# Optimization experiments

Hardware: AMD Instinct MI355X
Metric: run time of the kernel (lower is better)

## Reference

```python
import jax, jax.numpy as jnp
import numpy as np

N = 8192        # points
M = 131072      # query-key pairs (edges)
C_IN = 512
H = 8           # heads
D = 64          # head_channels
BINS = 48
BIN_SIZE = 0.05


def setup_inputs() -> dict:
    key = jax.random.key(0)
    ks = jax.random.split(key, 8)
    x_F = jax.random.normal(ks[0], (N, C_IN), dtype=jnp.float32)
    x_C = jax.random.uniform(ks[1], (N, 3), dtype=jnp.float32)
    qk_pair_idxs = jax.random.randint(ks[2], (2, M), 0, N, dtype=jnp.int64)
    W_qkv = jax.random.normal(ks[3], (C_IN, 3 * H * D), dtype=jnp.float32) * 0.02
    b_qkv = jnp.zeros((3 * H * D,), dtype=jnp.float32)
    q_tables = jax.random.normal(ks[4], (3, BINS, H, D), dtype=jnp.float32) * 0.02
    k_tables = jax.random.normal(ks[5], (3, BINS, H, D), dtype=jnp.float32) * 0.02
    v_tables = jax.random.normal(ks[6], (3, BINS, H, D), dtype=jnp.float32) * 0.02
    return {"x_F": x_F, "x_C": x_C, "qk_pair_idxs": qk_pair_idxs,
            "W_qkv": W_qkv, "b_qkv": b_qkv,
            "q_tables": q_tables, "k_tables": k_tables, "v_tables": v_tables}


def reference(x_F, x_C, qk_pair_idxs, W_qkv, b_qkv, q_tables, k_tables, v_tables):
    n = x_F.shape[0]
    qkv = (x_F @ W_qkv + b_qkv).reshape(n, 3, H, D)
    q = qkv[:, 0] * (D ** -0.5)   # scale folded into queries, as in the module
    k = qkv[:, 1]
    v = qkv[:, 2]
    qi = qk_pair_idxs[0]
    ki = qk_pair_idxs[1]
    # quantized relative coordinates -> table bin indices [M,3]
    rel = (x_C[qi] - x_C[ki]) / BIN_SIZE + BINS / 2
    idx = jnp.clip(rel.astype(jnp.int32), 0, BINS - 1)
    # precompute per-point, per-axis, per-bin table dot products [N,3,BINS,H]
    q_dot = jnp.einsum('nhd,abhd->nabh', q, q_tables)
    k_dot = jnp.einsum('nhd,abhd->nabh', k, k_tables)
    # content logits [M,H]
    logits = jnp.einsum('mhd,mhd->mh', q[qi], k[ki])
    for a in range(3):  # fixed xyz axes
        logits = logits + q_dot[qi, a, idx[:, a]] + k_dot[ki, a, idx[:, a]]
    # scatter softmax over query index (per head)
    seg_max = jax.ops.segment_max(logits, qi, num_segments=n)
    e = jnp.exp(logits - seg_max[qi])
    denom = jax.ops.segment_sum(e, qi, num_segments=n)
    attn = e / denom[qi]  # [M,H]
    # value-side relative position bias, summed over axes [M,H,D]
    vt = v_tables[0, idx[:, 0]] + v_tables[1, idx[:, 1]] + v_tables[2, idx[:, 2]]
    contrib = attn[:, :, None] * (v[ki] + vt)            # [M,H,D]
    agg = jax.ops.segment_sum(contrib, qi, num_segments=n)  # [N,H,D]
    return agg.reshape(n, H * D)
```

## Files before the change

### kernel.cpp

```cpp
#include <hip/hip_runtime.h>
#include <hip/hip_bf16.h>
#include <stdint.h>

#define N_PTS 8192
#define M_EDGES 131072
#define CIN 512
#define QKV_COLS 1536

typedef __bf16 bf16x8 __attribute__((ext_vector_type(8)));
typedef float f32x4 __attribute__((ext_vector_type(4)));

#define GAS __attribute__((address_space(1)))
#define LAS __attribute__((address_space(3)))

__device__ __forceinline__ void gload_lds16(const void* g, void* l) {
  __builtin_amdgcn_global_load_lds((const GAS void*)g, (LAS void*)l, 16, 0, 0);
}

__global__ void cast_a(const float* __restrict__ x, __bf16* __restrict__ a) {
  int i = blockIdx.x * blockDim.x + threadIdx.x;
  int base = i * 4;
  if (base < N_PTS * CIN) {
    float4 v = *(const float4*)(x + base);
    a[base + 0] = (__bf16)v.x;
    a[base + 1] = (__bf16)v.y;
    a[base + 2] = (__bf16)v.z;
    a[base + 3] = (__bf16)v.w;
  }
}

__global__ void cast_bt(const float* __restrict__ w, __bf16* __restrict__ bt) {
  __shared__ float tile[32][33];
  int bk = blockIdx.x, bn = blockIdx.y;
  int x = threadIdx.x & 31, y = threadIdx.x >> 5;
#pragma unroll
  for (int j = 0; j < 4; j++) {
    int r = y + j * 8;
    tile[r][x] = w[(size_t)(bk * 32 + r) * QKV_COLS + bn * 32 + x];
  }
  __syncthreads();
#pragma unroll
  for (int j = 0; j < 4; j++) {
    int r = y + j * 8;
    bt[(size_t)(bn * 32 + r) * CIN + bk * 32 + x] = (__bf16)tile[x][r];
  }
}

__global__ void cast_tables(const float* __restrict__ qt, const float* __restrict__ kt,
                            const float* __restrict__ vt, __bf16* __restrict__ qtb,
                            __bf16* __restrict__ ktb, __bf16* __restrict__ vtb) {
  int i = blockIdx.x * 256 + threadIdx.x;
  if (i >= 3 * 48 * 512) return;
  int d = i & 63, h = (i >> 6) & 7, ab = i >> 9;
  int po = (h * 144 + ab) * 64 + d;
  qtb[po] = (__bf16)qt[i];
  ktb[po] = (__bf16)kt[i];
  vtb[i] = (__bf16)vt[i];
}

__global__ __launch_bounds__(256) void gemm_qkv(const __bf16* __restrict__ A,
                                                const __bf16* __restrict__ BT,
                                                const float* __restrict__ bias,
                                                __bf16* __restrict__ qb,
                                                __bf16* __restrict__ kb,
                                                __bf16* __restrict__ vb) {
  __shared__ __align__(16) char At[128 * 32 * 2];
  __shared__ __align__(16) char Bt[128 * 32 * 2];
  int tid = threadIdx.x;
  int w = tid >> 6, l = tid & 63;
  int bm = blockIdx.x, bn = blockIdx.y;
  int wm = w & 1, wn = w >> 1;
  f32x4 acc[4][4] = {};
  const char* Ab = (const char*)A;
  const char* Bb = (const char*)BT;

  for (int kt = 0; kt < 16; kt++) {
#pragma unroll
    for (int r = 0; r < 2; r++) {
      int flat = r * 4096 + w * 1024 + l * 16;
      int row = flat >> 6, colb = flat & 63;
      gload_lds16(Ab + ((size_t)(bm * 128 + row) * CIN + kt * 32) * 2 + colb,
                  At + r * 4096 + w * 1024);
      gload_lds16(Bb + ((size_t)(bn * 128 + row) * CIN + kt * 32) * 2 + colb,
                  Bt + r * 4096 + w * 1024);
    }
    __syncthreads();
    bf16x8 af[4], bfr[4];
    int lr = l & 15;
    int lk = (l >> 4) * 16;
#pragma unroll
    for (int mf = 0; mf < 4; mf++) af[mf] = *(const bf16x8*)(At + (wm * 64 + mf * 16 + lr) * 64 + lk);
#pragma unroll
    for (int nf = 0; nf < 4; nf++) bfr[nf] = *(const bf16x8*)(Bt + (wn * 64 + nf * 16 + lr) * 64 + lk);
#pragma unroll
    for (int mf = 0; mf < 4; mf++)
#pragma unroll
      for (int nf = 0; nf < 4; nf++)
        acc[mf][nf] = __builtin_amdgcn_mfma_f32_16x16x32_bf16(af[mf], bfr[nf], acc[mf][nf], 0, 0, 0);
    __syncthreads();
  }

  int lr = l & 15, lg = l >> 4;
#pragma unroll
  for (int mf = 0; mf < 4; mf++) {
#pragma unroll
    for (int nf = 0; nf < 4; nf++) {
      int gc = bn * 128 + wn * 64 + nf * 16 + lr;
      float b = bias[gc];
      int which = gc >> 9;
      int col = gc & 511;
      __bf16* dst = which == 0 ? qb : (which == 1 ? kb : vb);
      float scale = which == 0 ? 0.125f : 1.0f;
#pragma unroll
      for (int j = 0; j < 4; j++) {
        int gr = bm * 128 + wm * 64 + mf * 16 + lg * 4 + j;
        dst[(size_t)gr * 512 + col] = (__bf16)((acc[mf][nf][j] + b) * scale);
      }
    }
  }
}

__global__ __launch_bounds__(256) void table_dot(const __bf16* __restrict__ src,
                                                 const __bf16* __restrict__ tab,
                                                 __bf16* __restrict__ out) {
  __shared__ __align__(16) char As[128 * 128];
  __shared__ __align__(16) char Bs[144 * 128];
  int nt = blockIdx.x, h = blockIdx.y;
  int tid = threadIdx.x, w = tid >> 6, l = tid & 63;
  const char* sb = (const char*)src;
  const char* tb = (const char*)tab + (size_t)h * 144 * 128;
#pragma unroll
  for (int p = 0; p < 4; p++) {
    int flat = p * 4096 + w * 1024 + l * 16;
    int row = flat >> 7, colb = flat & 127;
    gload_lds16(sb + (size_t)(nt * 128 + row) * 1024 + h * 128 + colb, As + p * 4096 + w * 1024);
    gload_lds16(tb + flat, Bs + p * 4096 + w * 1024);
  }
  if (w < 2) {
    int flat = 16384 + w * 1024 + l * 16;
    gload_lds16(tb + flat, Bs + 16384 + w * 1024);
  }
  __syncthreads();

  f32x4 acc[2][9] = {};
  int lr = l & 15, lk = (l >> 4) * 16;
#pragma unroll
  for (int ks = 0; ks < 2; ks++) {
    bf16x8 af[2], bf[9];
#pragma unroll
    for (int mf = 0; mf < 2; mf++)
      af[mf] = *(const bf16x8*)(As + (w * 32 + mf * 16 + lr) * 128 + ks * 64 + lk);
#pragma unroll
    for (int nf = 0; nf < 9; nf++)
      bf[nf] = *(const bf16x8*)(Bs + (nf * 16 + lr) * 128 + ks * 64 + lk);
#pragma unroll
    for (int mf = 0; mf < 2; mf++)
#pragma unroll
      for (int nf = 0; nf < 9; nf++)
        acc[mf][nf] = __builtin_amdgcn_mfma_f32_16x16x32_bf16(af[mf], bf[nf], acc[mf][nf], 0, 0, 0);
  }

  int lg = l >> 4;
#pragma unroll
  for (int mf = 0; mf < 2; mf++)
#pragma unroll
    for (int nf = 0; nf < 9; nf++)
#pragma unroll
      for (int j = 0; j < 4; j++) {
        int n = nt * 128 + w * 32 + mf * 16 + lg * 4 + j;
        int ab = nf * 16 + lr;
        out[(size_t)n * 1152 + ab * 8 + h] = (__bf16)acc[mf][nf][j];
      }
}

__global__ void edge_setup(const int* __restrict__ pairs, const float* __restrict__ xc,
                           int* __restrict__ qi_a, int* __restrict__ ki_a,
                           unsigned* __restrict__ bins, int* __restrict__ cnt) {
  int m = blockIdx.x * blockDim.x + threadIdx.x;
  if (m >= M_EDGES) return;
  int qi = pairs[m], ki = pairs[M_EDGES + m];
  unsigned pb = 0;
#pragma unroll
  for (int a = 0; a < 3; a++) {
    float rel = (xc[qi * 3 + a] - xc[ki * 3 + a]) / 0.05f + 24.0f;
    int b = (int)rel;
    b = b < 0 ? 0 : (b > 47 ? 47 : b);
    pb |= (unsigned)b << (6 * a);
  }
  qi_a[m] = qi;
  ki_a[m] = ki;
  bins[m] = pb;
  atomicAdd(&cnt[qi], 1);
}

__global__ __launch_bounds__(256) void scan_kernel(const int* __restrict__ cnt,
                                                   int* __restrict__ off,
                                                   int* __restrict__ cursor) {
  __shared__ int wsum[4];
  int tid = threadIdx.x, lane = tid & 63, w = tid >> 6;
  int local[32];
  int s = 0;
#pragma unroll
  for (int i = 0; i < 8; i++) {
    int4 v = ((const int4*)cnt)[tid * 8 + i];
    local[i * 4 + 0] = v.x; local[i * 4 + 1] = v.y;
    local[i * 4 + 2] = v.z; local[i * 4 + 3] = v.w;
    s += v.x + v.y + v.z + v.w;
  }
  int incl = s;
#pragma unroll
  for (int d = 1; d < 64; d <<= 1) {
    int t = __shfl_up(incl, d, 64);
    if (lane >= d) incl += t;
  }
  if (lane == 63) wsum[w] = incl;
  __syncthreads();
  int woff = 0;
#pragma unroll
  for (int j = 0; j < 4; j++) woff += (j < w) ? wsum[j] : 0;
  int run = woff + incl - s;
  int base = tid * 32;
#pragma unroll
  for (int i = 0; i < 32; i++) {
    off[base + i] = run;
    cursor[base + i] = run;
    run += local[i];
  }
  if (tid == 255) off[N_PTS] = run;
}

__global__ void scatter_k(const int* __restrict__ qi_a, const int* __restrict__ ki_a,
                          const unsigned* __restrict__ bins, int* __restrict__ cursor,
                          int* __restrict__ qi_s, int* __restrict__ ki_s,
                          unsigned* __restrict__ bins_s) {
  int m = blockIdx.x * blockDim.x + threadIdx.x;
  if (m < M_EDGES) {
    int qi = qi_a[m];
    int pos = atomicAdd(&cursor[qi], 1);
    qi_s[pos] = qi;
    ki_s[pos] = ki_a[m];
    bins_s[pos] = bins[m];
  }
}

__global__ void edge_bias(const int* __restrict__ qi_s, const int* __restrict__ ki_s,
                          const unsigned* __restrict__ bins_s, const __bf16* __restrict__ qdot,
                          const __bf16* __restrict__ kdot, float* __restrict__ eb) {
  int t = blockIdx.x * 256 + threadIdx.x;
  int e = t >> 3, h = t & 7;
  if (e >= M_EDGES) return;
  int qi = qi_s[e], ki = ki_s[e];
  unsigned pb = bins_s[e];
  int a0 = ((int)(pb & 63)) * 8 + h;
  int a1 = (48 + (int)((pb >> 6) & 63)) * 8 + h;
  int a2 = (96 + (int)((pb >> 12) & 63)) * 8 + h;
  const __bf16* qd = qdot + (size_t)qi * 1152;
  const __bf16* kd = kdot + (size_t)ki * 1152;
  eb[t] = (float)qd[a0] + (float)qd[a1] + (float)qd[a2] +
          (float)kd[a0] + (float)kd[a1] + (float)kd[a2];
}

__global__ __launch_bounds__(512) void attn_kernel(
    const __bf16* __restrict__ qb, const __bf16* __restrict__ kb,
    const __bf16* __restrict__ vb, const __bf16* __restrict__ vtb,
    const float* __restrict__ eb, const int* __restrict__ off,
    const int* __restrict__ ki_s, const unsigned* __restrict__ bins_s,
    float* __restrict__ out) {
  int n = blockIdx.x;
  int tid = threadIdx.x;
  int h = tid >> 6, l = tid & 63;
  int es = l >> 3;
  int dg = l & 7;
  int tcol = h * 64 + dg * 8;

  bf16x8 q8 = *(const bf16x8*)(qb + (size_t)n * 512 + tcol);
  float qv[8];
#pragma unroll
  for (int j = 0; j < 8; j++) qv[j] = (float)q8[j];

  float acc[8] = {0.f, 0.f, 0.f, 0.f, 0.f, 0.f, 0.f, 0.f};
  float den = 0.f;
  int e0 = off[n], e1 = off[n + 1];

  for (int base = e0; base < e1; base += 8) {
    int e = base + es;
    bool valid = e < e1;
    int ee = valid ? e : e0;
    int ki = ki_s[ee];
    unsigned pb = bins_s[ee];
    float ebv = eb[(size_t)ee * 8 + h];
    bf16x8 k8 = *(const bf16x8*)(kb + (size_t)ki * 512 + tcol);
    bf16x8 v8 = *(const bf16x8*)(vb + (size_t)ki * 512 + tcol);
    int b0 = pb & 63, b1 = (pb >> 6) & 63, b2 = (pb >> 12) & 63;
    bf16x8 t0 = *(const bf16x8*)(vtb + (size_t)b0 * 512 + tcol);
    bf16x8 t1 = *(const bf16x8*)(vtb + (size_t)(48 + b1) * 512 + tcol);
    bf16x8 t2 = *(const bf16x8*)(vtb + (size_t)(96 + b2) * 512 + tcol);
    float p = 0.f;
#pragma unroll
    for (int j = 0; j < 8; j++) p += qv[j] * (float)k8[j];
    p += __shfl_xor(p, 1, 64);
    p += __shfl_xor(p, 2, 64);
    p += __shfl_xor(p, 4, 64);
    p += ebv;
    float ex = valid ? __expf(p) : 0.f;
    den += ex;
#pragma unroll
    for (int j = 0; j < 8; j++)
      acc[j] += ex * ((float)v8[j] + (float)t0[j] + (float)t1[j] + (float)t2[j]);
  }

#pragma unroll
  for (int s = 8; s <= 32; s <<= 1) {
    den += __shfl_xor(den, s, 64);
#pragma unroll
    for (int j = 0; j < 8; j++) acc[j] += __shfl_xor(acc[j], s, 64);
  }

  if (l < 8) {
    float inv = (e1 > e0) ? 1.f / den : 0.f;
    float* op = out + (size_t)n * 512 + h * 64 + l * 8;
    f32x4 o0 = {acc[0] * inv, acc[1] * inv, acc[2] * inv, acc[3] * inv};
    f32x4 o1 = {acc[4] * inv, acc[5] * inv, acc[6] * inv, acc[7] * inv};
    *(f32x4*)op = o0;
    *(f32x4*)(op + 4) = o1;
  }
}

extern "C" void kernel_launch(void* const* d_in, const int* in_sizes, int n_in,
                              void* d_out, int out_size, void* d_ws, size_t ws_size,
                              hipStream_t stream) {
  const float* xF = (const float*)d_in[0];
  const float* xC = (const float*)d_in[1];
  const int* pairs = (const int*)d_in[2];
  const float* W = (const float*)d_in[3];
  const float* bias = (const float*)d_in[4];
  const float* qt = (const float*)d_in[5];
  const float* kt = (const float*)d_in[6];
  const float* vt = (const float*)d_in[7];
  float* out = (float*)d_out;

  char* ws = (char*)d_ws;
  size_t o = 0;
  auto alloc = [&](size_t bytes) {
    void* p = ws + o;
    o = (o + bytes + 255) & ~(size_t)255;
    return p;
  };
  __bf16* A = (__bf16*)alloc((size_t)N_PTS * CIN * 2);
  __bf16* BT = (__bf16*)alloc((size_t)QKV_COLS * CIN * 2);
  __bf16* qb = (__bf16*)alloc((size_t)N_PTS * 512 * 2);
  __bf16* kb = (__bf16*)alloc((size_t)N_PTS * 512 * 2);
  __bf16* vb = (__bf16*)alloc((size_t)N_PTS * 512 * 2);
  __bf16* qtb = (__bf16*)alloc((size_t)8 * 144 * 64 * 2);
  __bf16* ktb = (__bf16*)alloc((size_t)8 * 144 * 64 * 2);
  __bf16* vtb = (__bf16*)alloc((size_t)144 * 512 * 2);
  __bf16* qdot = (__bf16*)alloc((size_t)N_PTS * 1152 * 2);
  __bf16* kdot = (__bf16*)alloc((size_t)N_PTS * 1152 * 2);
  float* eb = (float*)alloc((size_t)M_EDGES * 8 * 4);
  int* qi_a = (int*)alloc(M_EDGES * 4);
  int* ki_a = (int*)alloc(M_EDGES * 4);
  unsigned* bins = (unsigned*)alloc(M_EDGES * 4);
  int* qi_s = (int*)alloc(M_EDGES * 4);
  int* ki_s = (int*)alloc(M_EDGES * 4);
  unsigned* bins_s = (unsigned*)alloc(M_EDGES * 4);
  int* cnt = (int*)alloc(N_PTS * 4);
  int* off = (int*)alloc((N_PTS + 1) * 4);
  int* cursor = (int*)alloc(N_PTS * 4);

  hipMemsetAsync(cnt, 0, N_PTS * 4, stream);

  cast_a<<<(N_PTS * CIN / 4 + 255) / 256, 256, 0, stream>>>(xF, A);
  cast_bt<<<dim3(CIN / 32, QKV_COLS / 32), 256, 0, stream>>>(W, BT);
  cast_tables<<<(3 * 48 * 512 + 255) / 256, 256, 0, stream>>>(qt, kt, vt, qtb, ktb, vtb);
  gemm_qkv<<<dim3(N_PTS / 128, QKV_COLS / 128), 256, 0, stream>>>(A, BT, bias, qb, kb, vb);
  table_dot<<<dim3(N_PTS / 128, 8), 256, 0, stream>>>(qb, qtb, qdot);
  table_dot<<<dim3(N_PTS / 128, 8), 256, 0, stream>>>(kb, ktb, kdot);
  edge_setup<<<M_EDGES / 256, 256, 0, stream>>>(pairs, xC, qi_a, ki_a, bins, cnt);
  scan_kernel<<<1, 256, 0, stream>>>(cnt, off, cursor);
  scatter_k<<<M_EDGES / 256, 256, 0, stream>>>(qi_a, ki_a, bins, cursor, qi_s, ki_s, bins_s);
  edge_bias<<<(M_EDGES * 8) / 256, 256, 0, stream>>>(qi_s, ki_s, bins_s, qdot, kdot, eb);
  attn_kernel<<<N_PTS, 512, 0, stream>>>(qb, kb, vb, vtb, eb, off, ki_s, bins_s, out);
}
```

Measured before the change: 172.0 us.

## Use persistent wave-per-(point,head) attention grid and read fp32 value tables directly

The attention kernel now launches a fixed grid of 1024 blocks. Each wave loops over (point, head) tasks in grid stride, rather than one block handling one point with all eight heads. The value tables are read in fp32 straight from the input, so the bf16 cast of v_tables and its workspace buffer are gone; this doubles the bytes per table gather. Several 64-bit index computations become 32-bit shifts to cut address arithmetic.

Result: slower. 246.3 us (+43.2%).

```diff
diff --git a/kernel.cpp b/kernel.cpp
--- a/kernel.cpp
+++ b/kernel.cpp
@@ -9,6 +9,7 @@
 
 typedef __bf16 bf16x8 __attribute__((ext_vector_type(8)));
 typedef float f32x4 __attribute__((ext_vector_type(4)));
+typedef float f32x8 __attribute__((ext_vector_type(8)));
 
 #define GAS __attribute__((address_space(1)))
 #define LAS __attribute__((address_space(3)))
@@ -47,15 +48,13 @@
 }
 
 __global__ void cast_tables(const float* __restrict__ qt, const float* __restrict__ kt,
-                            const float* __restrict__ vt, __bf16* __restrict__ qtb,
-                            __bf16* __restrict__ ktb, __bf16* __restrict__ vtb) {
+                            __bf16* __restrict__ qtb, __bf16* __restrict__ ktb) {
   int i = blockIdx.x * 256 + threadIdx.x;
   if (i >= 3 * 48 * 512) return;
   int d = i & 63, h = (i >> 6) & 7, ab = i >> 9;
   int po = (h * 144 + ab) * 64 + d;
   qtb[po] = (__bf16)qt[i];
   ktb[po] = (__bf16)kt[i];
-  vtb[i] = (__bf16)vt[i];
 }
 
 __global__ __launch_bounds__(256) void gemm_qkv(const __bf16* __restrict__ A,
@@ -254,75 +253,81 @@
   int a0 = ((int)(pb & 63)) * 8 + h;
   int a1 = (48 + (int)((pb >> 6) & 63)) * 8 + h;
   int a2 = (96 + (int)((pb >> 12) & 63)) * 8 + h;
-  const __bf16* qd = qdot + (size_t)qi * 1152;
-  const __bf16* kd = kdot + (size_t)ki * 1152;
+  const __bf16* qd = qdot + qi * 1152;
+  const __bf16* kd = kdot + ki * 1152;
   eb[t] = (float)qd[a0] + (float)qd[a1] + (float)qd[a2] +
           (float)kd[a0] + (float)kd[a1] + (float)kd[a2];
 }
 
+#define ATTN_BLOCKS 1024
 __global__ __launch_bounds__(512) void attn_kernel(
     const __bf16* __restrict__ qb, const __bf16* __restrict__ kb,
-    const __bf16* __restrict__ vb, const __bf16* __restrict__ vtb,
+    const __bf16* __restrict__ vb, const float* __restrict__ vt,
     const float* __restrict__ eb, const int* __restrict__ off,
     const int* __restrict__ ki_s, const unsigned* __restrict__ bins_s,
     float* __restrict__ out) {
-  int n = blockIdx.x;
   int tid = threadIdx.x;
-  int h = tid >> 6, l = tid & 63;
+  int w = tid >> 6, l = tid & 63;
   int es = l >> 3;
   int dg = l & 7;
-  int tcol = h * 64 + dg * 8;
-
-  bf16x8 q8 = *(const bf16x8*)(qb + (size_t)n * 512 + tcol);
-  float qv[8];
-#pragma unroll
-  for (int j = 0; j < 8; j++) qv[j] = (float)q8[j];
-
-  float acc[8] = {0.f, 0.f, 0.f, 0.f, 0.f, 0.f, 0.f, 0.f};
-  float den = 0.f;
-  int e0 = off[n], e1 = off[n + 1];
-
-  for (int base = e0; base < e1; base += 8) {
-    int e = base + es;
-    bool valid = e < e1;
-    int ee = valid ? e : e0;
-    int ki = ki_s[ee];
-    unsigned pb = bins_s[ee];
-    float ebv = eb[(size_t)ee * 8 + h];
-    bf16x8 k8 = *(const bf16x8*)(kb + (size_t)ki * 512 + tcol);
-    bf16x8 v8 = *(const bf16x8*)(vb + (size_t)ki * 512 + tcol);
-    int b0 = pb & 63, b1 = (pb >> 6) & 63, b2 = (pb >> 12) & 63;
-    bf16x8 t0 = *(const bf16x8*)(vtb + (size_t)b0 * 512 + tcol);
-    bf16x8 t1 = *(const bf16x8*)(vtb + (size_t)(48 + b1) * 512 + tcol);
-    bf16x8 t2 = *(const bf16x8*)(vtb + (size_t)(96 + b2) * 512 + tcol);
-    float p = 0.f;
-#pragma unroll
-    for (int j = 0; j < 8; j++) p += qv[j] * (float)k8[j];
-    p += __shfl_xor(p, 1, 64);
-    p += __shfl_xor(p, 2, 64);
-    p += __shfl_xor(p, 4, 64);
-    p += ebv;
-    float ex = valid ? __expf(p) : 0.f;
-    den += ex;
-#pragma unroll
-    for (int j = 0; j < 8; j++)
-      acc[j] += ex * ((float)v8[j] + (float)t0[j] + (float)t1[j] + (float)t2[j]);
-  }
-
-#pragma unroll
-  for (int s = 8; s <= 32; s <<= 1) {
-    den += __shfl_xor(den, s, 64);
-#pragma unroll
-    for (int j = 0; j < 8; j++) acc[j] += __shfl_xor(acc[j], s, 64);
-  }
-
-  if (l < 8) {
-    float inv = (e1 > e0) ? 1.f / den : 0.f;
-    float* op = out + (size_t)n * 512 + h * 64 + l * 8;
-    f32x4 o0 = {acc[0] * inv, acc[1] * inv, acc[2] * inv, acc[3] * inv};
-    f32x4 o1 = {acc[4] * inv, acc[5] * inv, acc[6] * inv, acc[7] * inv};
-    *(f32x4*)op = o0;
-    *(f32x4*)(op + 4) = o1;
+  int gwave = blockIdx.x * 8 + w;
+
+  for (int task = gwave; task < N_PTS * 8; task += ATTN_BLOCKS * 8) {
+    int n = task >> 3;
+    int h = task & 7;
+    int tcol = h * 64 + dg * 8;
+
+    bf16x8 q8 = *(const bf16x8*)(qb + (n << 9) + tcol);
+    float qv[8];
+#pragma unroll
+    for (int j = 0; j < 8; j++) qv[j] = (float)q8[j];
+
+    float acc[8] = {0.f, 0.f, 0.f, 0.f, 0.f, 0.f, 0.f, 0.f};
+    float den = 0.f;
+    int e0 = off[n], e1 = off[n + 1];
+
+    for (int base = e0; base < e1; base += 8) {
+      int e = base + es;
+      bool valid = e < e1;
+      int ee = valid ? e : e0;
+      int ki = ki_s[ee];
+      unsigned pb = bins_s[ee];
+      float ebv = eb[(ee << 3) + h];
+      bf16x8 k8 = *(const bf16x8*)(kb + (ki << 9) + tcol);
+      bf16x8 v8 = *(const bf16x8*)(vb + (ki << 9) + tcol);
+      int b0 = pb & 63, b1 = (pb >> 6) & 63, b2 = (pb >> 12) & 63;
+      f32x8 t0 = *(const f32x8*)(vt + (b0 << 9) + tcol);
+      f32x8 t1 = *(const f32x8*)(vt + ((48 + b1) << 9) + tcol);
+      f32x8 t2 = *(const f32x8*)(vt + ((96 + b2) << 9) + tcol);
+      float p = 0.f;
+#pragma unroll
+      for (int j = 0; j < 8; j++) p += qv[j] * (float)k8[j];
+      p += __shfl_xor(p, 1, 64);
+      p += __shfl_xor(p, 2, 64);
+      p += __shfl_xor(p, 4, 64);
+      p += ebv;
+      float ex = valid ? __expf(p) : 0.f;
+      den += ex;
+#pragma unroll
+      for (int j = 0; j < 8; j++)
+        acc[j] += ex * ((float)v8[j] + t0[j] + t1[j] + t2[j]);
+    }
+
+#pragma unroll
+    for (int s = 8; s <= 32; s <<= 1) {
+      den += __shfl_xor(den, s, 64);
+#pragma unroll
+      for (int j = 0; j < 8; j++) acc[j] += __shfl_xor(acc[j], s, 64);
+    }
+
+    if (es == 0) {
+      float inv = (e1 > e0) ? 1.f / den : 0.f;
+      float* op = out + (n << 9) + h * 64 + dg * 8;
+      f32x4 o0 = {acc[0] * inv, acc[1] * inv, acc[2] * inv, acc[3] * inv};
+      f32x4 o1 = {acc[4] * inv, acc[5] * inv, acc[6] * inv, acc[7] * inv};
+      *(f32x4*)op = o0;
+      *(f32x4*)(op + 4) = o1;
+    }
   }
 }
 
@@ -353,7 +358,6 @@
   __bf16* vb = (__bf16*)alloc((size_t)N_PTS * 512 * 2);
   __bf16* qtb = (__bf16*)alloc((size_t)8 * 144 * 64 * 2);
   __bf16* ktb = (__bf16*)alloc((size_t)8 * 144 * 64 * 2);
-  __bf16* vtb = (__bf16*)alloc((size_t)144 * 512 * 2);
   __bf16* qdot = (__bf16*)alloc((size_t)N_PTS * 1152 * 2);
   __bf16* kdot = (__bf16*)alloc((size_t)N_PTS * 1152 * 2);
   float* eb = (float*)alloc((size_t)M_EDGES * 8 * 4);
@@ -371,7 +375,7 @@
 
   cast_a<<<(N_PTS * CIN / 4 + 255) / 256, 256, 0, stream>>>(xF, A);
   cast_bt<<<dim3(CIN / 32, QKV_COLS / 32), 256, 0, stream>>>(W, BT);
-  cast_tables<<<(3 * 48 * 512 + 255) / 256, 256, 0, stream>>>(qt, kt, vt, qtb, ktb, vtb);
+  cast_tables<<<(3 * 48 * 512 + 255) / 256, 256, 0, stream>>>(qt, kt, qtb, ktb);
   gemm_qkv<<<dim3(N_PTS / 128, QKV_COLS / 128), 256, 0, stream>>>(A, BT, bias, qb, kb, vb);
   table_dot<<<dim3(N_PTS / 128, 8), 256, 0, stream>>>(qb, qtb, qdot);
   table_dot<<<dim3(N_PTS / 128, 8), 256, 0, stream>>>(kb, ktb, kdot);
@@ -379,5 +383,5 @@
   scan_kernel<<<1, 256, 0, stream>>>(cnt, off, cursor);
   scatter_k<<<M_EDGES / 256, 256, 0, stream>>>(qi_a, ki_a, bins, cursor, qi_s, ki_s, bins_s);
   edge_bias<<<(M_EDGES * 8) / 256, 256, 0, stream>>>(qi_s, ki_s, bins_s, qdot, kdot, eb);
-  attn_kernel<<<N_PTS, 512, 0, stream>>>(qb, kb, vb, vtb, eb, off, ki_s, bins_s, out);
-}
+  attn_kernel<<<ATTN_BLOCKS, 512, 0, stream>>>(qb, kb, vb, vt, eb, off, ki_s, bins_s, out);
+}
```
